# Performance work log

Measured on AMD Instinct MI355X. Metric: run time of the kernel, lower is better.

Reference implementation:

```python
import jax, jax.numpy as jnp
import numpy as np

B, T, C = 4, 2048, 1024
N_HEAD = 16
HEAD_DIM = C // N_HEAD


def setup_inputs() -> dict:
    key = jax.random.key(0)
    k1, k2, k3 = jax.random.split(key, 3)
    x = jax.random.normal(k1, (B, T, C), dtype=jnp.float32)
    # Linear weights stored as (in, out); scaled like typical init
    w_qkv = jax.random.normal(k2, (C, 3 * C), dtype=jnp.float32) * (1.0 / np.sqrt(C))
    w_proj = jax.random.normal(k3, (C, C), dtype=jnp.float32) * (1.0 / np.sqrt(C))
    return {"x": x, "w_qkv": w_qkv, "w_proj": w_proj}


def reference(x, w_qkv, w_proj):
    b, t, c = x.shape
    qkv = x @ w_qkv                      # (B,T,3C)
    q, k, v = jnp.split(qkv, 3, axis=-1)
    # (B,H,T,D)
    def to_heads(a):
        return a.reshape(b, t, N_HEAD, HEAD_DIM).transpose(0, 2, 1, 3)
    q, k, v = to_heads(q), to_heads(k), to_heads(v)
    scale = 1.0 / np.sqrt(HEAD_DIM).astype(np.float32)
    att = jnp.einsum('bhqd,bhkd->bhqk', q, k) * scale   # (B,H,T,T)
    causal = jnp.tril(jnp.ones((t, t), dtype=bool))
    att = jnp.where(causal[None, None, :, :], att, -jnp.inf)
    att = jax.nn.softmax(att, axis=-1)
    # dropout p=0.0 (eval) -> identity
    y = jnp.einsum('bhqk,bhkd->bhqd', att, v)            # (B,H,T,D)
    y = y.transpose(0, 2, 1, 3).reshape(b, t, c)
    return y @ w_proj
```

## Files before the change

### kernel.cpp

```cpp
#include <hip/hip_runtime.h>
#include <hip/hip_bf16.h>
#include <stdint.h>

#define Bsz 4
#define Tsz 2048
#define Csz 1024
#define Hn  16
#define Dh  64
#define BH  (Bsz*Hn)
#define Mrows (Bsz*Tsz)
#define N1  (3*Csz)

typedef short s16x8 __attribute__((ext_vector_type(8)));
typedef short s16x4 __attribute__((ext_vector_type(4)));
typedef float fx4   __attribute__((ext_vector_type(4)));

static __device__ __forceinline__ short f2bf(float x) {
  __hip_bfloat16 h = __float2bfloat16(x);
  return __builtin_bit_cast(short, h);
}

#define GLDS16(g, l) __builtin_amdgcn_global_load_lds( \
    (const __attribute__((address_space(1))) void*)(g), \
    (__attribute__((address_space(3))) void*)(l), 16, 0, 0)

__global__ void cvt_kernel(const float* __restrict__ in, short* __restrict__ out, int n4) {
  int i = blockIdx.x * blockDim.x + threadIdx.x;
  int stride = blockDim.x * gridDim.x;
  for (; i < n4; i += stride) {
    float4 v = ((const float4*)in)[i];
    s16x4 o;
    o.x = f2bf(v.x); o.y = f2bf(v.y); o.z = f2bf(v.z); o.w = f2bf(v.w);
    ((s16x4*)out)[i] = o;
  }
}

__global__ void transpose_cvt_kernel(const float* __restrict__ w, short* __restrict__ wt,
                                     int K, int N) {
  __shared__ float tile[32][33];
  int tc = threadIdx.x & 31;
  int tr = threadIdx.x >> 5;
  int n0 = blockIdx.x * 32;
  int k0 = blockIdx.y * 32;
#pragma unroll
  for (int p = 0; p < 4; p++) {
    int r = tr + p*8;
    tile[r][tc] = w[(size_t)(k0 + r) * N + (n0 + tc)];
  }
  __syncthreads();
#pragma unroll
  for (int p = 0; p < 4; p++) {
    int r = tr + p*8;
    wt[(size_t)(n0 + r) * K + (k0 + tc)] = f2bf(tile[tc][r]);
  }
}

static __device__ __forceinline__ s16x8 lds_frag(const short* p, int off) {
  return *(const s16x8*)(p + off);
}

__global__ __launch_bounds__(512) void gemm_bt_kernel(
    const short* __restrict__ A, const short* __restrict__ Bt,
    float* __restrict__ Cf,
    short* __restrict__ Qo, short* __restrict__ Ko, short* __restrict__ Vo,
    int Mdim, int Ndim, int Kdim, int mode)
{
  __shared__ __align__(16) short sA[3][128*64];
  __shared__ __align__(16) short sB[3][256*64];
  const int tid  = threadIdx.x;
  const int lane = tid & 63;
  const int lr   = lane & 15;
  const int lq   = lane >> 4;
  const int wv   = tid >> 6;
  const int nb   = Ndim >> 8;
  const int nwg  = (int)gridDim.x;
  const int orig = (int)blockIdx.x;
  const int wgid = (orig & 7) * (nwg >> 3) + (orig >> 3);
  const int bm   = wgid / nb;
  const int bn   = wgid % nb;
  const int m_off = (wv & 1) << 6;
  const int n_off = (wv >> 1) << 6;

  const short* Ab = A  + (size_t)bm * 128 * Kdim;
  const short* Bb = Bt + (size_t)bn * 256 * Kdim;

  const short* gA[2];
  const short* gB[4];
#pragma unroll
  for (int j = 0; j < 2; j++) {
    int c = tid + 512*j, r = c >> 3, o = ((c & 7) ^ (r & 7)) * 8;
    gA[j] = Ab + (size_t)r * Kdim + o;
  }
#pragma unroll
  for (int j = 0; j < 4; j++) {
    int c = tid + 512*j, r = c >> 3, o = ((c & 7) ^ (r & 7)) * 8;
    gB[j] = Bb + (size_t)r * Kdim + o;
  }

  int offA[4][2], offB[4][2];
#pragma unroll
  for (int ft = 0; ft < 4; ft++)
#pragma unroll
    for (int kk = 0; kk < 2; kk++) {
      int ra = m_off + ft*16 + lr;
      offA[ft][kk] = ra*64 + ((((kk<<2) | lq) ^ (ra & 7)) << 3);
      int rb = n_off + ft*16 + lr;
      offB[ft][kk] = rb*64 + ((((kk<<2) | lq) ^ (rb & 7)) << 3);
    }

  fx4 acc[4][4];
#pragma unroll
  for (int i = 0; i < 4; i++)
#pragma unroll
    for (int j = 0; j < 4; j++) acc[i][j] = (fx4){0.f, 0.f, 0.f, 0.f};

  auto STAGE_P1 = [&](int k0, short* dA, short* dB) {
    GLDS16(gA[0] + k0, dA + tid*8);
    GLDS16(gA[1] + k0, dA + (tid+512)*8);
    GLDS16(gB[0] + k0, dB + tid*8);
  };
  auto STAGE_P2 = [&](int k0, short* dB) {
    GLDS16(gB[1] + k0, dB + (tid+512)*8);
    GLDS16(gB[2] + k0, dB + (tid+1024)*8);
    GLDS16(gB[3] + k0, dB + (tid+1536)*8);
  };

  const int NIT = Kdim >> 6;

  STAGE_P1(0,  sA[0], sB[0]); STAGE_P2(0,  sB[0]);
  STAGE_P1(64, sA[1], sB[1]); STAGE_P2(64, sB[1]);
  __asm__ __volatile__("s_waitcnt vmcnt(6)" ::: "memory");
  __builtin_amdgcn_s_barrier();

  const short *cA = sA[0], *cB = sB[0];
  const short *nA = sA[1], *nB = sB[1];
  short *eA = sA[2], *eB = sB[2];

  for (int t = 0; t < NIT; ++t) {
    if (t + 2 < NIT) STAGE_P1((t+2)*64, eA, eB);

    s16x8 af[4][2], bf[2][2];
#pragma unroll
    for (int mt = 0; mt < 4; mt++)
#pragma unroll
      for (int kk = 0; kk < 2; kk++)
        af[mt][kk] = lds_frag(cA, offA[mt][kk]);
#pragma unroll
    for (int nt = 0; nt < 2; nt++)
#pragma unroll
      for (int kk = 0; kk < 2; kk++)
        bf[nt][kk] = lds_frag(cB, offB[nt][kk]);
    __builtin_amdgcn_s_setprio(1);
#pragma unroll
    for (int kk = 0; kk < 2; kk++)
#pragma unroll
      for (int mt = 0; mt < 4; mt++) {
        acc[mt][0] = __builtin_amdgcn_mfma_f32_16x16x32_bf16(af[mt][kk], bf[0][kk], acc[mt][0], 0, 0, 0);
        acc[mt][1] = __builtin_amdgcn_mfma_f32_16x16x32_bf16(af[mt][kk], bf[1][kk], acc[mt][1], 0, 0, 0);
      }
    __builtin_amdgcn_s_setprio(0);
    __builtin_amdgcn_sched_barrier(0);
    __builtin_amdgcn_s_barrier();

    if (t + 2 < NIT) STAGE_P2((t+2)*64, eB);
#pragma unroll
    for (int nt = 0; nt < 2; nt++)
#pragma unroll
      for (int kk = 0; kk < 2; kk++)
        bf[nt][kk] = lds_frag(cB, offB[nt+2][kk]);
    __builtin_amdgcn_s_setprio(1);
#pragma unroll
    for (int kk = 0; kk < 2; kk++)
#pragma unroll
      for (int mt = 0; mt < 4; mt++) {
        acc[mt][2] = __builtin_amdgcn_mfma_f32_16x16x32_bf16(af[mt][kk], bf[0][kk], acc[mt][2], 0, 0, 0);
        acc[mt][3] = __builtin_amdgcn_mfma_f32_16x16x32_bf16(af[mt][kk], bf[1][kk], acc[mt][3], 0, 0, 0);
      }
    __builtin_amdgcn_s_setprio(0);
    __builtin_amdgcn_sched_barrier(0);
    if (t + 2 < NIT) {
      __asm__ __volatile__("s_waitcnt vmcnt(6)" ::: "memory");
    } else if (t + 1 < NIT) {
      __asm__ __volatile__("s_waitcnt vmcnt(0)" ::: "memory");
    }
    __builtin_amdgcn_s_barrier();

    const short *tAp = cA, *tBp = cB;
    cA = nA; cB = nB;
    nA = eA; nB = eB;
    eA = (short*)tAp; eB = (short*)tBp;
  }

  const int gm0 = bm*128 + m_off;
  const int gn0 = bn*256 + n_off;
  if (mode == 0) {
#pragma unroll
    for (int mt = 0; mt < 4; mt++)
#pragma unroll
      for (int nt = 0; nt < 4; nt++) {
        int col = gn0 + nt*16 + lr;
#pragma unroll
        for (int r = 0; r < 4; r++) {
          int row = gm0 + mt*16 + lq*4 + r;
          Cf[(size_t)row * Ndim + col] = acc[mt][nt][r];
        }
      }
  } else {
#pragma unroll
    for (int mt = 0; mt < 4; mt++)
#pragma unroll
      for (int nt = 0; nt < 4; nt++) {
        int n   = gn0 + nt*16 + lr;
        int sec = n >> 10;
        int cc  = n & 1023;
        int hh  = cc >> 6;
        int dd  = cc & 63;
        if (sec == 2) {
          int tt0 = gm0 + mt*16 + lq*4;
          int bb  = tt0 >> 11;
          int bh  = bb * Hn + hh;
          s16x4 pk;
          pk.x = f2bf(acc[mt][nt][0]); pk.y = f2bf(acc[mt][nt][1]);
          pk.z = f2bf(acc[mt][nt][2]); pk.w = f2bf(acc[mt][nt][3]);
          *(s16x4*)(Vo + ((size_t)bh * Dh + dd) * Tsz + (tt0 & 2047)) = pk;
        } else {
#pragma unroll
          for (int r = 0; r < 4; r++) {
            int m  = gm0 + mt*16 + lq*4 + r;
            int bb = m >> 11;
            int tt = m & 2047;
            int bh = bb * Hn + hh;
            short v = f2bf(acc[mt][nt][r]);
            if (sec == 0) Qo[((size_t)bh * Tsz + tt) * Dh + dd] = v;
            else          Ko[((size_t)bh * Tsz + tt) * Dh + dd] = v;
          }
        }
      }
  }
}

#define PPITCH 72

static __device__ __forceinline__ void attn_stage(
    const short* __restrict__ Kp, const short* __restrict__ Vp, int kbase,
    short* __restrict__ sK, short* __restrict__ sV,
    int c0, int r0, int g0, int c1, int r1, int g1)
{
  GLDS16(Kp + (size_t)(kbase + r0)*Dh + g0, sK + c0*8);
  GLDS16(Kp + (size_t)(kbase + r1)*Dh + g1, sK + c1*8);
  GLDS16(Vp + (size_t)r0*Tsz + kbase + g0, sV + c0*8);
  GLDS16(Vp + (size_t)r1*Tsz + kbase + g1, sV + c1*8);
}

static __device__ __forceinline__ void attn_compute(
    const short* __restrict__ sK, const short* __restrict__ sV,
    int kbase, int q0, int lr, int lq, int sw,
    short* __restrict__ pb, const s16x8 bq[2][2], fx4 o[2][4], float li[2])
{
  const float sc = 0.125f * 1.44269504f;
  const bool masked = (kbase + 63 > q0);

  fx4 s[2][4];
#pragma unroll
  for (int j = 0; j < 2; j++)
#pragma unroll
    for (int mt = 0; mt < 4; mt++) s[j][mt] = (fx4){0.f,0.f,0.f,0.f};
#pragma unroll
  for (int mt = 0; mt < 4; mt++)
#pragma unroll
    for (int kk = 0; kk < 2; kk++) {
      const s16x8 akf = *(const s16x8*)(sK + (mt*16 + lr)*64 + ((kk*4 + lq) ^ sw)*8);
      s[0][mt] = __builtin_amdgcn_mfma_f32_16x16x32_bf16(akf, bq[0][kk], s[0][mt], 0, 0, 0);
      s[1][mt] = __builtin_amdgcn_mfma_f32_16x16x32_bf16(akf, bq[1][kk], s[1][mt], 0, 0, 0);
    }

#pragma unroll
  for (int j = 0; j < 2; j++) {
    const int qg = q0 + 16*j + lr;
    float p[16];
#pragma unroll
    for (int mt = 0; mt < 4; mt++)
#pragma unroll
      for (int r = 0; r < 4; r++) {
        float v = s[j][mt][r];
        if (masked) {
          int jg = kbase + mt*16 + lq*4 + r;
          v = (jg <= qg) ? v : -1e30f;
        }
        p[mt*4 + r] = __builtin_amdgcn_exp2f(v * sc);
      }
    float s8[8];
#pragma unroll
    for (int i = 0; i < 8; i++) s8[i] = p[i] + p[i+8];
    float s4[4];
#pragma unroll
    for (int i = 0; i < 4; i++) s4[i] = s8[i] + s8[i+4];
    li[j] += (s4[0] + s4[2]) + (s4[1] + s4[3]);
#pragma unroll
    for (int mt = 0; mt < 4; mt++) {
      s16x4 pk;
      pk.x = f2bf(p[mt*4+0]); pk.y = f2bf(p[mt*4+1]);
      pk.z = f2bf(p[mt*4+2]); pk.w = f2bf(p[mt*4+3]);
      *(s16x4*)(pb + (16*j + lr)*PPITCH + mt*16 + lq*4) = pk;
    }
  }
  __asm__ __volatile__("" ::: "memory");
  s16x8 pf[2][2];
#pragma unroll
  for (int j = 0; j < 2; j++)
#pragma unroll
    for (int kk = 0; kk < 2; kk++)
      pf[j][kk] = *(const s16x8*)(pb + (16*j + lr)*PPITCH + kk*32 + lq*8);
  __asm__ __volatile__("" ::: "memory");

#pragma unroll
  for (int dt = 0; dt < 4; dt++)
#pragma unroll
    for (int kk = 0; kk < 2; kk++) {
      const s16x8 avf = *(const s16x8*)(sV + (dt*16 + lr)*64 + ((kk*4 + lq) ^ sw)*8);
      o[0][dt] = __builtin_amdgcn_mfma_f32_16x16x32_bf16(avf, pf[0][kk], o[0][dt], 0, 0, 0);
      o[1][dt] = __builtin_amdgcn_mfma_f32_16x16x32_bf16(avf, pf[1][kk], o[1][dt], 0, 0, 0);
    }
}

__global__ __launch_bounds__(256) void attn_kernel(
    const short* __restrict__ Qb, const short* __restrict__ Kb,
    const short* __restrict__ Vt, short* __restrict__ Y)
{
  __shared__ __align__(16) short sK[2][64*64];
  __shared__ __align__(16) short sV[2][64*64];
  __shared__ __align__(16) short pbuf[4][32*PPITCH];
  const int tid  = threadIdx.x;
  const int lane = tid & 63;
  const int wv   = tid >> 6;
  const int lr   = lane & 15;
  const int lq   = lane >> 4;
  const int sw   = lr & 7;
  const int bh   = blockIdx.x;
  const int qb   = 15 - (int)blockIdx.y;
  const int b    = bh >> 4;
  const int h    = bh & 15;
  const int q0   = qb*128 + wv*32;

  const short* Qp = Qb + (size_t)bh * Tsz * Dh;
  const short* Kp = Kb + (size_t)bh * Tsz * Dh;
  const short* Vp = Vt + (size_t)bh * Dh * Tsz;
  short* pb = pbuf[wv];

  const int c0 = tid,       r0 = c0 >> 3, g0 = (((c0 & 7) ^ (r0 & 7)) * 8);
  const int c1 = tid + 256, r1 = c1 >> 3, g1 = (((c1 & 7) ^ (r1 & 7)) * 8);

  s16x8 bq[2][2];
#pragma unroll
  for (int j = 0; j < 2; j++)
#pragma unroll
    for (int kk = 0; kk < 2; kk++)
      bq[j][kk] = *(const s16x8*)(Qp + (size_t)(q0 + 16*j + lr)*Dh + kk*32 + lq*8);

  fx4 o[2][4];
#pragma unroll
  for (int j = 0; j < 2; j++)
#pragma unroll
    for (int i = 0; i < 4; i++) o[j][i] = (fx4){0.f, 0.f, 0.f, 0.f};
  float li[2] = {0.f, 0.f};

  const int ntiles = 2*qb + 2;
  attn_stage(Kp, Vp, 0, sK[0], sV[0], c0, r0, g0, c1, r1, g1);
  for (int kt = 0; kt < ntiles; kt += 2) {
    __syncthreads();
    if (kt + 1 < ntiles) attn_stage(Kp, Vp, (kt+1)*64, sK[1], sV[1], c0, r0, g0, c1, r1, g1);
    if (kt*64 <= q0 + 31)
      attn_compute(sK[0], sV[0], kt*64, q0, lr, lq, sw, pb, bq, o, li);
    __syncthreads();
    if (kt + 2 < ntiles) attn_stage(Kp, Vp, (kt+2)*64, sK[0], sV[0], c0, r0, g0, c1, r1, g1);
    if ((kt+1)*64 <= q0 + 31)
      attn_compute(sK[1], sV[1], (kt+1)*64, q0, lr, lq, sw, pb, bq, o, li);
  }

#pragma unroll
  for (int j = 0; j < 2; j++) {
    float l = li[j];
    l += __shfl_xor(l, 16);
    l += __shfl_xor(l, 32);
    float inv = 1.0f / l;
#pragma unroll
    for (int dt = 0; dt < 4; dt++) {
      s16x4 yk;
      yk.x = f2bf(o[j][dt][0]*inv); yk.y = f2bf(o[j][dt][1]*inv);
      yk.z = f2bf(o[j][dt][2]*inv); yk.w = f2bf(o[j][dt][3]*inv);
      *(s16x4*)(Y + ((size_t)b*Tsz + q0 + 16*j + lr)*Csz + h*Dh + dt*16 + lq*4) = yk;
    }
  }
}

extern "C" void kernel_launch(void* const* d_in, const int* in_sizes, int n_in,
                              void* d_out, int out_size, void* d_ws, size_t ws_size,
                              hipStream_t stream)
{
  const float* x  = (const float*)d_in[0];
  const float* wq = (const float*)d_in[1];
  const float* wp = (const float*)d_in[2];
  float* out = (float*)d_out;

  char* ws = (char*)d_ws;
  size_t off = 0;
  short* xb  = (short*)(ws + off); off += (size_t)Mrows*Csz*2;
  short* wqT = (short*)(ws + off); off += (size_t)N1*Csz*2;
  short* wpT = (short*)(ws + off); off += (size_t)Csz*Csz*2;
  short* Qb  = (short*)(ws + off); off += (size_t)BH*Tsz*Dh*2;
  short* Kb  = (short*)(ws + off); off += (size_t)BH*Tsz*Dh*2;
  short* Vt  = (short*)(ws + off); off += (size_t)BH*Dh*Tsz*2;
  short* Yb  = (short*)(ws + off); off += (size_t)Mrows*Csz*2;

  cvt_kernel<<<1024, 256, 0, stream>>>(x, xb, Mrows*Csz/4);
  transpose_cvt_kernel<<<dim3(N1/32, Csz/32), 256, 0, stream>>>(wq, wqT, Csz, N1);
  transpose_cvt_kernel<<<dim3(Csz/32, Csz/32), 256, 0, stream>>>(wp, wpT, Csz, Csz);
  gemm_bt_kernel<<<(Mrows/128)*(N1/256), 512, 0, stream>>>(
      xb, wqT, nullptr, Qb, Kb, Vt, Mrows, N1, Csz, 1);
  attn_kernel<<<dim3(BH, Tsz/128), 256, 0, stream>>>(Qb, Kb, Vt, Yb);
  gemm_bt_kernel<<<(Mrows/128)*(Csz/256), 512, 0, stream>>>(
      Yb, wpT, out, nullptr, nullptr, nullptr, Mrows, Csz, Csz, 0);
}
```

Measured before the change: 254.8 us.

## Enlarge GEMM tile to 256x256 with 4-stage K=32 LDS pipeline

Restructures the bf16 GEMM used for the QKV and output projections. Tiles grow from 128x256 to 256x256 per workgroup, with each wave owning a 128x64 sub-tile. The K step shrinks to 32 and becomes a 4-buffer ring with 3 stages in flight, and the LDS swizzle is changed to match. The aim is more operand reuse per loaded byte and better latency hiding, at the cost of more accumulator registers, half as many workgroups (lower occupancy and wave-count balance), and more barriers per unit of K.

```diff
diff --git a/kernel.cpp b/kernel.cpp
--- a/kernel.cpp
+++ b/kernel.cpp
@@ -59,143 +59,136 @@
   return *(const s16x8*)(p + off);
 }
 
+#define TILE_SH 8192
+
 __global__ __launch_bounds__(512) void gemm_bt_kernel(
     const short* __restrict__ A, const short* __restrict__ Bt,
     float* __restrict__ Cf,
     short* __restrict__ Qo, short* __restrict__ Ko, short* __restrict__ Vo,
     int Mdim, int Ndim, int Kdim, int mode)
 {
-  __shared__ __align__(16) short sA[3][128*64];
-  __shared__ __align__(16) short sB[3][256*64];
+  __shared__ __align__(16) short sA4[4*TILE_SH];
+  __shared__ __align__(16) short sB4[4*TILE_SH];
   const int tid  = threadIdx.x;
   const int lane = tid & 63;
   const int lr   = lane & 15;
   const int lq   = lane >> 4;
   const int wv   = tid >> 6;
+  const int wm   = wv >> 2;
+  const int wn   = wv & 3;
   const int nb   = Ndim >> 8;
   const int nwg  = (int)gridDim.x;
   const int orig = (int)blockIdx.x;
   const int wgid = (orig & 7) * (nwg >> 3) + (orig >> 3);
   const int bm   = wgid / nb;
   const int bn   = wgid % nb;
-  const int m_off = (wv & 1) << 6;
-  const int n_off = (wv >> 1) << 6;
-
-  const short* Ab = A  + (size_t)bm * 128 * Kdim;
+
+  const short* Ab = A  + (size_t)bm * 256 * Kdim;
   const short* Bb = Bt + (size_t)bn * 256 * Kdim;
 
-  const short* gA[2];
-  const short* gB[4];
-#pragma unroll
-  for (int j = 0; j < 2; j++) {
-    int c = tid + 512*j, r = c >> 3, o = ((c & 7) ^ (r & 7)) * 8;
-    gA[j] = Ab + (size_t)r * Kdim + o;
-  }
-#pragma unroll
-  for (int j = 0; j < 4; j++) {
-    int c = tid + 512*j, r = c >> 3, o = ((c & 7) ^ (r & 7)) * 8;
-    gB[j] = Bb + (size_t)r * Kdim + o;
-  }
-
-  int offA[4][2], offB[4][2];
-#pragma unroll
-  for (int ft = 0; ft < 4; ft++)
-#pragma unroll
-    for (int kk = 0; kk < 2; kk++) {
-      int ra = m_off + ft*16 + lr;
-      offA[ft][kk] = ra*64 + ((((kk<<2) | lq) ^ (ra & 7)) << 3);
-      int rb = n_off + ft*16 + lr;
-      offB[ft][kk] = rb*64 + ((((kk<<2) | lq) ^ (rb & 7)) << 3);
-    }
-
-  fx4 acc[4][4];
-#pragma unroll
-  for (int i = 0; i < 4; i++)
+  const int rr0 = tid >> 2,        ss0 = ((tid & 3) ^ ((rr0 >> 1) & 3)) * 8;
+  const int rr1 = rr0 + 128,       ss1 = ((tid & 3) ^ ((rr1 >> 1) & 3)) * 8;
+  const short* gA0 = Ab + (size_t)rr0 * Kdim + ss0;
+  const short* gA1 = Ab + (size_t)rr1 * Kdim + ss1;
+  const short* gB0 = Bb + (size_t)rr0 * Kdim + ss0;
+  const short* gB1 = Bb + (size_t)rr1 * Kdim + ss1;
+
+  int offA[8], offB[4];
+#pragma unroll
+  for (int mt = 0; mt < 8; mt++) {
+    int row = wm*128 + mt*16 + lr;
+    offA[mt] = row*32 + ((lq ^ ((row >> 1) & 3)) << 3);
+  }
+#pragma unroll
+  for (int nt = 0; nt < 4; nt++) {
+    int row = wn*64 + nt*16 + lr;
+    offB[nt] = row*32 + ((lq ^ ((row >> 1) & 3)) << 3);
+  }
+
+  fx4 acc[8][4];
+#pragma unroll
+  for (int i = 0; i < 8; i++)
 #pragma unroll
     for (int j = 0; j < 4; j++) acc[i][j] = (fx4){0.f, 0.f, 0.f, 0.f};
 
-  auto STAGE_P1 = [&](int k0, short* dA, short* dB) {
-    GLDS16(gA[0] + k0, dA + tid*8);
-    GLDS16(gA[1] + k0, dA + (tid+512)*8);
-    GLDS16(gB[0] + k0, dB + tid*8);
-  };
-  auto STAGE_P2 = [&](int k0, short* dB) {
-    GLDS16(gB[1] + k0, dB + (tid+512)*8);
-    GLDS16(gB[2] + k0, dB + (tid+1024)*8);
-    GLDS16(gB[3] + k0, dB + (tid+1536)*8);
-  };
-
-  const int NIT = Kdim >> 6;
-
-  STAGE_P1(0,  sA[0], sB[0]); STAGE_P2(0,  sB[0]);
-  STAGE_P1(64, sA[1], sB[1]); STAGE_P2(64, sB[1]);
-  __asm__ __volatile__("s_waitcnt vmcnt(6)" ::: "memory");
+  const int NIT = Kdim >> 5;
+
+#pragma unroll
+  for (int k = 0; k < 3; k++) {
+    short* dA = sA4 + k*TILE_SH;
+    short* dB = sB4 + k*TILE_SH;
+    GLDS16(gA0 + k*32, dA + tid*8);
+    GLDS16(gA1 + k*32, dA + (tid+512)*8);
+    GLDS16(gB0 + k*32, dB + tid*8);
+    GLDS16(gB1 + k*32, dB + (tid+512)*8);
+  }
+  __asm__ __volatile__("s_waitcnt vmcnt(8)" ::: "memory");
   __builtin_amdgcn_s_barrier();
-
-  const short *cA = sA[0], *cB = sB[0];
-  const short *nA = sA[1], *nB = sB[1];
-  short *eA = sA[2], *eB = sB[2];
+  __builtin_amdgcn_sched_barrier(0);
 
   for (int t = 0; t < NIT; ++t) {
-    if (t + 2 < NIT) STAGE_P1((t+2)*64, eA, eB);
-
-    s16x8 af[4][2], bf[2][2];
+    const short* cA = sA4 + (t & 3)*TILE_SH;
+    const short* cB = sB4 + (t & 3)*TILE_SH;
+    short* eA = sA4 + ((t + 3) & 3)*TILE_SH;
+    short* eB = sB4 + ((t + 3) & 3)*TILE_SH;
+    const bool pre = (t + 3 < NIT);
+
+    s16x8 bfr[4], afr[4];
+#pragma unroll
+    for (int nt = 0; nt < 4; nt++) bfr[nt] = lds_frag(cB, offB[nt]);
+#pragma unroll
+    for (int mt = 0; mt < 4; mt++) afr[mt] = lds_frag(cA, offA[mt]);
+    if (pre) {
+      GLDS16(gA0 + (t+3)*32, eA + tid*8);
+      GLDS16(gA1 + (t+3)*32, eA + (tid+512)*8);
+    }
+    __builtin_amdgcn_s_barrier();
+    __asm__ __volatile__("s_waitcnt lgkmcnt(0)" ::: "memory");
+    __builtin_amdgcn_sched_barrier(0);
+    __builtin_amdgcn_s_setprio(1);
 #pragma unroll
     for (int mt = 0; mt < 4; mt++)
 #pragma unroll
-      for (int kk = 0; kk < 2; kk++)
-        af[mt][kk] = lds_frag(cA, offA[mt][kk]);
-#pragma unroll
-    for (int nt = 0; nt < 2; nt++)
-#pragma unroll
-      for (int kk = 0; kk < 2; kk++)
-        bf[nt][kk] = lds_frag(cB, offB[nt][kk]);
+      for (int nt = 0; nt < 4; nt++)
+        acc[mt][nt] = __builtin_amdgcn_mfma_f32_16x16x32_bf16(afr[mt], bfr[nt], acc[mt][nt], 0, 0, 0);
+    __builtin_amdgcn_s_setprio(0);
+    __builtin_amdgcn_sched_barrier(0);
+    __builtin_amdgcn_s_barrier();
+    __builtin_amdgcn_sched_barrier(0);
+
+#pragma unroll
+    for (int mt = 0; mt < 4; mt++) afr[mt] = lds_frag(cA, offA[mt+4]);
+    if (pre) {
+      GLDS16(gB0 + (t+3)*32, eB + tid*8);
+      GLDS16(gB1 + (t+3)*32, eB + (tid+512)*8);
+    }
+    __builtin_amdgcn_s_barrier();
+    __asm__ __volatile__("s_waitcnt lgkmcnt(0)" ::: "memory");
+    __builtin_amdgcn_sched_barrier(0);
     __builtin_amdgcn_s_setprio(1);
 #pragma unroll
-    for (int kk = 0; kk < 2; kk++)
-#pragma unroll
-      for (int mt = 0; mt < 4; mt++) {
-        acc[mt][0] = __builtin_amdgcn_mfma_f32_16x16x32_bf16(af[mt][kk], bf[0][kk], acc[mt][0], 0, 0, 0);
-        acc[mt][1] = __builtin_amdgcn_mfma_f32_16x16x32_bf16(af[mt][kk], bf[1][kk], acc[mt][1], 0, 0, 0);
-      }
+    for (int mt = 0; mt < 4; mt++)
+#pragma unroll
+      for (int nt = 0; nt < 4; nt++)
+        acc[mt+4][nt] = __builtin_amdgcn_mfma_f32_16x16x32_bf16(afr[mt], bfr[nt], acc[mt+4][nt], 0, 0, 0);
     __builtin_amdgcn_s_setprio(0);
     __builtin_amdgcn_sched_barrier(0);
-    __builtin_amdgcn_s_barrier();
-
-    if (t + 2 < NIT) STAGE_P2((t+2)*64, eB);
-#pragma unroll
-    for (int nt = 0; nt < 2; nt++)
-#pragma unroll
-      for (int kk = 0; kk < 2; kk++)
-        bf[nt][kk] = lds_frag(cB, offB[nt+2][kk]);
-    __builtin_amdgcn_s_setprio(1);
-#pragma unroll
-    for (int kk = 0; kk < 2; kk++)
-#pragma unroll
-      for (int mt = 0; mt < 4; mt++) {
-        acc[mt][2] = __builtin_amdgcn_mfma_f32_16x16x32_bf16(af[mt][kk], bf[0][kk], acc[mt][2], 0, 0, 0);
-        acc[mt][3] = __builtin_amdgcn_mfma_f32_16x16x32_bf16(af[mt][kk], bf[1][kk], acc[mt][3], 0, 0, 0);
-      }
-    __builtin_amdgcn_s_setprio(0);
-    __builtin_amdgcn_sched_barrier(0);
-    if (t + 2 < NIT) {
-      __asm__ __volatile__("s_waitcnt vmcnt(6)" ::: "memory");
+    if (t + 3 < NIT) {
+      __asm__ __volatile__("s_waitcnt vmcnt(8)" ::: "memory");
+    } else if (t + 2 < NIT) {
+      __asm__ __volatile__("s_waitcnt vmcnt(4)" ::: "memory");
     } else if (t + 1 < NIT) {
       __asm__ __volatile__("s_waitcnt vmcnt(0)" ::: "memory");
     }
     __builtin_amdgcn_s_barrier();
-
-    const short *tAp = cA, *tBp = cB;
-    cA = nA; cB = nB;
-    nA = eA; nB = eB;
-    eA = (short*)tAp; eB = (short*)tBp;
-  }
-
-  const int gm0 = bm*128 + m_off;
-  const int gn0 = bn*256 + n_off;
+    __builtin_amdgcn_sched_barrier(0);
+  }
+
+  const int gm0 = bm*256 + wm*128;
+  const int gn0 = bn*256 + wn*64;
   if (mode == 0) {
 #pragma unroll
-    for (int mt = 0; mt < 4; mt++)
+    for (int mt = 0; mt < 8; mt++)
 #pragma unroll
       for (int nt = 0; nt < 4; nt++) {
         int col = gn0 + nt*16 + lr;
@@ -207,7 +200,7 @@
       }
   } else {
 #pragma unroll
-    for (int mt = 0; mt < 4; mt++)
+    for (int mt = 0; mt < 8; mt++)
 #pragma unroll
       for (int nt = 0; nt < 4; nt++) {
         int n   = gn0 + nt*16 + lr;
@@ -415,9 +408,9 @@
   cvt_kernel<<<1024, 256, 0, stream>>>(x, xb, Mrows*Csz/4);
   transpose_cvt_kernel<<<dim3(N1/32, Csz/32), 256, 0, stream>>>(wq, wqT, Csz, N1);
   transpose_cvt_kernel<<<dim3(Csz/32, Csz/32), 256, 0, stream>>>(wp, wpT, Csz, Csz);
-  gemm_bt_kernel<<<(Mrows/128)*(N1/256), 512, 0, stream>>>(
+  gemm_bt_kernel<<<(Mrows/256)*(N1/256), 512, 0, stream>>>(
       xb, wqT, nullptr, Qb, Kb, Vt, Mrows, N1, Csz, 1);
   attn_kernel<<<dim3(BH, Tsz/128), 256, 0, stream>>>(Qb, Kb, Vt, Yb);
-  gemm_bt_kernel<<<(Mrows/128)*(Csz/256), 512, 0, stream>>>(
+  gemm_bt_kernel<<<(Mrows/256)*(Csz/256), 512, 0, stream>>>(
       Yb, wpT, out, nullptr, nullptr, nullptr, Mrows, Csz, Csz, 0);
 }
```

Result: slower. 263.7 us (+3.5%).

## Add 256x256 QKV GEMM with 4-stage pipeline and widen attention blocks to 256 queries

Applied to the files above, without the earlier changes.

Adds a new QKV projection GEMM kernel that uses 256x256 output tiles with a K-step of 32 and a four-buffer LDS pipeline. This raises data reuse per workgroup and reduces the tile count. The attention kernel now runs 512 threads (8 waves) per block covering 256 queries, so each K/V tile loaded to LDS is shared by twice as many waves. It also reorders the query-block schedule and wraps the MFMA sections in raised wave priority. The trade-offs are fewer workgroups (possible occupancy or load-balance loss) and higher register pressure from the 8x4 accumulator tile.

```diff
diff --git a/kernel.cpp b/kernel.cpp
--- a/kernel.cpp
+++ b/kernel.cpp
@@ -59,7 +59,178 @@
   return *(const s16x8*)(p + off);
 }
 
-__global__ __launch_bounds__(512) void gemm_bt_kernel(
+#define WAITV(n) __asm__ __volatile__("s_waitcnt vmcnt(" #n ")" ::: "memory")
+
+#define TILE_SH 8192
+
+__global__ __launch_bounds__(512) void gemm_bt256_kernel(
+    const short* __restrict__ A, const short* __restrict__ Bt,
+    float* __restrict__ Cf,
+    short* __restrict__ Qo, short* __restrict__ Ko, short* __restrict__ Vo,
+    int Mdim, int Ndim, int Kdim, int mode)
+{
+  __shared__ __align__(16) short sA4[4*TILE_SH];
+  __shared__ __align__(16) short sB4[4*TILE_SH];
+  const int tid  = threadIdx.x;
+  const int lane = tid & 63;
+  const int lr   = lane & 15;
+  const int lq   = lane >> 4;
+  const int wv   = tid >> 6;
+  const int wm   = wv >> 2;
+  const int wn   = wv & 3;
+  const int nb   = Ndim >> 8;
+  const int nwg  = (int)gridDim.x;
+  const int orig = (int)blockIdx.x;
+  const int wgid = (orig & 7) * (nwg >> 3) + (orig >> 3);
+  const int bm   = wgid / nb;
+  const int bn   = wgid % nb;
+
+  const short* Ab = A  + (size_t)bm * 256 * Kdim;
+  const short* Bb = Bt + (size_t)bn * 256 * Kdim;
+
+  const int rr0 = tid >> 2,        ss0 = ((tid & 3) ^ ((rr0 >> 1) & 3)) * 8;
+  const int rr1 = rr0 + 128,       ss1 = ((tid & 3) ^ ((rr1 >> 1) & 3)) * 8;
+  const short* gA0 = Ab + (size_t)rr0 * Kdim + ss0;
+  const short* gA1 = Ab + (size_t)rr1 * Kdim + ss1;
+  const short* gB0 = Bb + (size_t)rr0 * Kdim + ss0;
+  const short* gB1 = Bb + (size_t)rr1 * Kdim + ss1;
+
+  int offA[8], offB[4];
+#pragma unroll
+  for (int mt = 0; mt < 8; mt++) {
+    int row = wm*128 + mt*16 + lr;
+    offA[mt] = row*32 + ((lq ^ ((row >> 1) & 3)) << 3);
+  }
+#pragma unroll
+  for (int nt = 0; nt < 4; nt++) {
+    int row = wn*64 + nt*16 + lr;
+    offB[nt] = row*32 + ((lq ^ ((row >> 1) & 3)) << 3);
+  }
+
+  fx4 acc[8][4];
+#pragma unroll
+  for (int i = 0; i < 8; i++)
+#pragma unroll
+    for (int j = 0; j < 4; j++) acc[i][j] = (fx4){0.f, 0.f, 0.f, 0.f};
+
+  const int NIT = Kdim >> 5;
+
+#pragma unroll
+  for (int k = 0; k < 3; k++) {
+    short* dA = sA4 + k*TILE_SH;
+    short* dB = sB4 + k*TILE_SH;
+    GLDS16(gA0 + k*32, dA + tid*8);
+    GLDS16(gA1 + k*32, dA + (tid+512)*8);
+    GLDS16(gB0 + k*32, dB + tid*8);
+    GLDS16(gB1 + k*32, dB + (tid+512)*8);
+  }
+  WAITV(8);
+  __builtin_amdgcn_s_barrier();
+  __builtin_amdgcn_sched_barrier(0);
+
+  for (int t = 0; t < NIT; ++t) {
+    const short* cA = sA4 + (t & 3)*TILE_SH;
+    const short* cB = sB4 + (t & 3)*TILE_SH;
+    short* eA = sA4 + ((t + 3) & 3)*TILE_SH;
+    short* eB = sB4 + ((t + 3) & 3)*TILE_SH;
+    const bool pre = (t + 3 < NIT);
+
+    s16x8 bfr[4], afr[4];
+#pragma unroll
+    for (int nt = 0; nt < 4; nt++) bfr[nt] = lds_frag(cB, offB[nt]);
+#pragma unroll
+    for (int mt = 0; mt < 4; mt++) afr[mt] = lds_frag(cA, offA[mt]);
+    if (pre) {
+      GLDS16(gA0 + (t+3)*32, eA + tid*8);
+      GLDS16(gA1 + (t+3)*32, eA + (tid+512)*8);
+    }
+    __builtin_amdgcn_s_barrier();
+    __asm__ __volatile__("s_waitcnt lgkmcnt(0)" ::: "memory");
+    __builtin_amdgcn_sched_barrier(0);
+    __builtin_amdgcn_s_setprio(1);
+#pragma unroll
+    for (int mt = 0; mt < 4; mt++)
+#pragma unroll
+      for (int nt = 0; nt < 4; nt++)
+        acc[mt][nt] = __builtin_amdgcn_mfma_f32_16x16x32_bf16(afr[mt], bfr[nt], acc[mt][nt], 0, 0, 0);
+    __builtin_amdgcn_s_setprio(0);
+    __builtin_amdgcn_sched_barrier(0);
+    __builtin_amdgcn_s_barrier();
+    __builtin_amdgcn_sched_barrier(0);
+
+#pragma unroll
+    for (int mt = 0; mt < 4; mt++) afr[mt] = lds_frag(cA, offA[mt+4]);
+    if (pre) {
+      GLDS16(gB0 + (t+3)*32, eB + tid*8);
+      GLDS16(gB1 + (t+3)*32, eB + (tid+512)*8);
+    }
+    __builtin_amdgcn_s_barrier();
+    __asm__ __volatile__("s_waitcnt lgkmcnt(0)" ::: "memory");
+    __builtin_amdgcn_sched_barrier(0);
+    __builtin_amdgcn_s_setprio(1);
+#pragma unroll
+    for (int mt = 0; mt < 4; mt++)
+#pragma unroll
+      for (int nt = 0; nt < 4; nt++)
+        acc[mt+4][nt] = __builtin_amdgcn_mfma_f32_16x16x32_bf16(afr[mt], bfr[nt], acc[mt+4][nt], 0, 0, 0);
+    __builtin_amdgcn_s_setprio(0);
+    __builtin_amdgcn_sched_barrier(0);
+    if (t + 3 < NIT)      { WAITV(8); }
+    else if (t + 2 < NIT) { WAITV(4); }
+    else if (t + 1 < NIT) { WAITV(0); }
+    __builtin_amdgcn_s_barrier();
+    __builtin_amdgcn_sched_barrier(0);
+  }
+
+  const int gm0 = bm*256 + wm*128;
+  const int gn0 = bn*256 + wn*64;
+  if (mode == 0) {
+#pragma unroll
+    for (int mt = 0; mt < 8; mt++)
+#pragma unroll
+      for (int nt = 0; nt < 4; nt++) {
+        int col = gn0 + nt*16 + lr;
+#pragma unroll
+        for (int r = 0; r < 4; r++) {
+          int row = gm0 + mt*16 + lq*4 + r;
+          Cf[(size_t)row * Ndim + col] = acc[mt][nt][r];
+        }
+      }
+  } else {
+#pragma unroll
+    for (int mt = 0; mt < 8; mt++)
+#pragma unroll
+      for (int nt = 0; nt < 4; nt++) {
+        int n   = gn0 + nt*16 + lr;
+        int sec = n >> 10;
+        int cc  = n & 1023;
+        int hh  = cc >> 6;
+        int dd  = cc & 63;
+        if (sec == 2) {
+          int tt0 = gm0 + mt*16 + lq*4;
+          int bb  = tt0 >> 11;
+          int bh  = bb * Hn + hh;
+          s16x4 pk;
+          pk.x = f2bf(acc[mt][nt][0]); pk.y = f2bf(acc[mt][nt][1]);
+          pk.z = f2bf(acc[mt][nt][2]); pk.w = f2bf(acc[mt][nt][3]);
+          *(s16x4*)(Vo + ((size_t)bh * Dh + dd) * Tsz + (tt0 & 2047)) = pk;
+        } else {
+#pragma unroll
+          for (int r = 0; r < 4; r++) {
+            int m  = gm0 + mt*16 + lq*4 + r;
+            int bb = m >> 11;
+            int tt = m & 2047;
+            int bh = bb * Hn + hh;
+            short v = f2bf(acc[mt][nt][r]);
+            if (sec == 0) Qo[((size_t)bh * Tsz + tt) * Dh + dd] = v;
+            else          Ko[((size_t)bh * Tsz + tt) * Dh + dd] = v;
+          }
+        }
+      }
+  }
+}
+
+__global__ __launch_bounds__(512) void gemm_bt128_kernel(
     const short* __restrict__ A, const short* __restrict__ Bt,
     float* __restrict__ Cf,
     short* __restrict__ Qo, short* __restrict__ Ko, short* __restrict__ Vo,
@@ -129,7 +300,7 @@
 
   STAGE_P1(0,  sA[0], sB[0]); STAGE_P2(0,  sB[0]);
   STAGE_P1(64, sA[1], sB[1]); STAGE_P2(64, sB[1]);
-  __asm__ __volatile__("s_waitcnt vmcnt(6)" ::: "memory");
+  WAITV(6);
   __builtin_amdgcn_s_barrier();
 
   const short *cA = sA[0], *cB = sB[0];
@@ -178,11 +349,8 @@
       }
     __builtin_amdgcn_s_setprio(0);
     __builtin_amdgcn_sched_barrier(0);
-    if (t + 2 < NIT) {
-      __asm__ __volatile__("s_waitcnt vmcnt(6)" ::: "memory");
-    } else if (t + 1 < NIT) {
-      __asm__ __volatile__("s_waitcnt vmcnt(0)" ::: "memory");
-    }
+    if (t + 2 < NIT)      { WAITV(6); }
+    else if (t + 1 < NIT) { WAITV(0); }
     __builtin_amdgcn_s_barrier();
 
     const short *tAp = cA, *tBp = cB;
@@ -244,12 +412,10 @@
 static __device__ __forceinline__ void attn_stage(
     const short* __restrict__ Kp, const short* __restrict__ Vp, int kbase,
     short* __restrict__ sK, short* __restrict__ sV,
-    int c0, int r0, int g0, int c1, int r1, int g1)
+    int c0, int r0, int g0)
 {
   GLDS16(Kp + (size_t)(kbase + r0)*Dh + g0, sK + c0*8);
-  GLDS16(Kp + (size_t)(kbase + r1)*Dh + g1, sK + c1*8);
   GLDS16(Vp + (size_t)r0*Tsz + kbase + g0, sV + c0*8);
-  GLDS16(Vp + (size_t)r1*Tsz + kbase + g1, sV + c1*8);
 }
 
 static __device__ __forceinline__ void attn_compute(
@@ -265,6 +431,7 @@
   for (int j = 0; j < 2; j++)
 #pragma unroll
     for (int mt = 0; mt < 4; mt++) s[j][mt] = (fx4){0.f,0.f,0.f,0.f};
+  __builtin_amdgcn_s_setprio(1);
 #pragma unroll
   for (int mt = 0; mt < 4; mt++)
 #pragma unroll
@@ -273,6 +440,7 @@
       s[0][mt] = __builtin_amdgcn_mfma_f32_16x16x32_bf16(akf, bq[0][kk], s[0][mt], 0, 0, 0);
       s[1][mt] = __builtin_amdgcn_mfma_f32_16x16x32_bf16(akf, bq[1][kk], s[1][mt], 0, 0, 0);
     }
+  __builtin_amdgcn_s_setprio(0);
 
 #pragma unroll
   for (int j = 0; j < 2; j++) {
@@ -313,6 +481,7 @@
       pf[j][kk] = *(const s16x8*)(pb + (16*j + lr)*PPITCH + kk*32 + lq*8);
   __asm__ __volatile__("" ::: "memory");
 
+  __builtin_amdgcn_s_setprio(1);
 #pragma unroll
   for (int dt = 0; dt < 4; dt++)
 #pragma unroll
@@ -321,15 +490,16 @@
       o[0][dt] = __builtin_amdgcn_mfma_f32_16x16x32_bf16(avf, pf[0][kk], o[0][dt], 0, 0, 0);
       o[1][dt] = __builtin_amdgcn_mfma_f32_16x16x32_bf16(avf, pf[1][kk], o[1][dt], 0, 0, 0);
     }
-}
-
-__global__ __launch_bounds__(256) void attn_kernel(
+  __builtin_amdgcn_s_setprio(0);
+}
+
+__global__ __launch_bounds__(512) void attn_kernel(
     const short* __restrict__ Qb, const short* __restrict__ Kb,
     const short* __restrict__ Vt, short* __restrict__ Y)
 {
   __shared__ __align__(16) short sK[2][64*64];
   __shared__ __align__(16) short sV[2][64*64];
-  __shared__ __align__(16) short pbuf[4][32*PPITCH];
+  __shared__ __align__(16) short pbuf[8][32*PPITCH];
   const int tid  = threadIdx.x;
   const int lane = tid & 63;
   const int wv   = tid >> 6;
@@ -337,18 +507,18 @@
   const int lq   = lane >> 4;
   const int sw   = lr & 7;
   const int bh   = blockIdx.x;
-  const int qb   = 15 - (int)blockIdx.y;
+  const int y    = (int)blockIdx.y;
+  const int qb   = (y < 4) ? (7 - y) : (y - 4);
   const int b    = bh >> 4;
   const int h    = bh & 15;
-  const int q0   = qb*128 + wv*32;
+  const int q0   = qb*256 + wv*32;
 
   const short* Qp = Qb + (size_t)bh * Tsz * Dh;
   const short* Kp = Kb + (size_t)bh * Tsz * Dh;
   const short* Vp = Vt + (size_t)bh * Dh * Tsz;
   short* pb = pbuf[wv];
 
-  const int c0 = tid,       r0 = c0 >> 3, g0 = (((c0 & 7) ^ (r0 & 7)) * 8);
-  const int c1 = tid + 256, r1 = c1 >> 3, g1 = (((c1 & 7) ^ (r1 & 7)) * 8);
+  const int c0 = tid, r0 = c0 >> 3, g0 = (((c0 & 7) ^ (r0 & 7)) * 8);
 
   s16x8 bq[2][2];
 #pragma unroll
@@ -364,15 +534,15 @@
     for (int i = 0; i < 4; i++) o[j][i] = (fx4){0.f, 0.f, 0.f, 0.f};
   float li[2] = {0.f, 0.f};
 
-  const int ntiles = 2*qb + 2;
-  attn_stage(Kp, Vp, 0, sK[0], sV[0], c0, r0, g0, c1, r1, g1);
+  const int ntiles = 4*qb + 4;
+  attn_stage(Kp, Vp, 0, sK[0], sV[0], c0, r0, g0);
   for (int kt = 0; kt < ntiles; kt += 2) {
     __syncthreads();
-    if (kt + 1 < ntiles) attn_stage(Kp, Vp, (kt+1)*64, sK[1], sV[1], c0, r0, g0, c1, r1, g1);
+    if (kt + 1 < ntiles) attn_stage(Kp, Vp, (kt+1)*64, sK[1], sV[1], c0, r0, g0);
     if (kt*64 <= q0 + 31)
       attn_compute(sK[0], sV[0], kt*64, q0, lr, lq, sw, pb, bq, o, li);
     __syncthreads();
-    if (kt + 2 < ntiles) attn_stage(Kp, Vp, (kt+2)*64, sK[0], sV[0], c0, r0, g0, c1, r1, g1);
+    if (kt + 2 < ntiles) attn_stage(Kp, Vp, (kt+2)*64, sK[0], sV[0], c0, r0, g0);
     if ((kt+1)*64 <= q0 + 31)
       attn_compute(sK[1], sV[1], (kt+1)*64, q0, lr, lq, sw, pb, bq, o, li);
   }
@@ -415,9 +585,9 @@
   cvt_kernel<<<1024, 256, 0, stream>>>(x, xb, Mrows*Csz/4);
   transpose_cvt_kernel<<<dim3(N1/32, Csz/32), 256, 0, stream>>>(wq, wqT, Csz, N1);
   transpose_cvt_kernel<<<dim3(Csz/32, Csz/32), 256, 0, stream>>>(wp, wpT, Csz, Csz);
-  gemm_bt_kernel<<<(Mrows/128)*(N1/256), 512, 0, stream>>>(
+  gemm_bt256_kernel<<<(Mrows/256)*(N1/256), 512, 0, stream>>>(
       xb, wqT, nullptr, Qb, Kb, Vt, Mrows, N1, Csz, 1);
-  attn_kernel<<<dim3(BH, Tsz/128), 256, 0, stream>>>(Qb, Kb, Vt, Yb);
-  gemm_bt_kernel<<<(Mrows/128)*(Csz/256), 512, 0, stream>>>(
+  attn_kernel<<<dim3(BH, Tsz/256), 512, 0, stream>>>(Qb, Kb, Vt, Yb);
+  gemm_bt128_kernel<<<(Mrows/128)*(Csz/256), 512, 0, stream>>>(
       Yb, wpT, out, nullptr, nullptr, nullptr, Mrows, Csz, Csz, 0);
 }
```

Measured after the change: 268.6 us. +5.4%, slower.
